# Kernel optimization log

Measured on AMD Instinct MI355X. Metric: run time of the kernel, lower is better.

The kernel has to match this reference:

```python
import math
import jax, jax.numpy as jnp
import numpy as np

B, N, D, H = 2, 8192, 1024, 16


def setup_inputs() -> dict:
    key = jax.random.key(0)
    k1, k2, k3, k4 = jax.random.split(key, 4)
    s = 1.0 / math.sqrt(D)
    return {
        "x": jax.random.normal(k1, (B, N, D), dtype=jnp.float32),
        "W_qk": jax.random.normal(k2, (D, D), dtype=jnp.float32) * s,
        "W_v": jax.random.normal(k3, (D, D), dtype=jnp.float32) * s,
        "W_out": jax.random.normal(k4, (D, D), dtype=jnp.float32) * s,
        "tau": jnp.ones((H, 1, 1), dtype=jnp.float32),
    }


def reference(x, W_qk, W_v, W_out, tau):
    b, n, d = x.shape
    h = H
    dh = d // h
    # QK / V projections (no bias), then to channel-major (B, H, dh, N)
    qk = (x @ W_qk).transpose(0, 2, 1).reshape(b, h, dh, n)
    v = (x @ W_v).transpose(0, 2, 1).reshape(b, h, dh, n)
    # Cross-channel Gram matrix over tokens: (B, H, dh, dh)
    dot = jnp.einsum('bhcn,bhdn->bhcd', qk, qk)
    q2 = jnp.sum(qk * qk, axis=-1)  # (B, H, dh)
    # Negative squared Euclidean distance between channel vectors
    logits = (2.0 * dot - q2[:, :, :, None] - q2[:, :, None, :]) / math.sqrt(max(n, 1))
    logits = logits * tau[None, ...]
    attn = jax.nn.softmax(logits, axis=-1)  # (B, H, dh, dh)
    w = jnp.einsum('bhcd,bhdn->bhcn', attn, v)  # (B, H, dh, N)
    out = w.reshape(b, d, n).transpose(0, 2, 1) @ W_out  # (B, N, D)
    return out
```

## Files before the change

kernel.cpp:

```cpp
#include <hip/hip_runtime.h>
#include <hip/hip_bf16.h>
#include <cstdint>
#include <cstddef>

typedef __bf16 v8bf __attribute__((ext_vector_type(8)));
typedef float  v4f  __attribute__((ext_vector_type(4)));

__device__ __forceinline__ unsigned short f2bf(float f) {
    unsigned int u = __float_as_uint(f);
    u += 0x7fffu + ((u >> 16) & 1u);
    return (unsigned short)(u >> 16);
}

__device__ __forceinline__ void gload_lds16(const unsigned short* g, unsigned short* l) {
    __builtin_amdgcn_global_load_lds(
        (const __attribute__((address_space(1))) unsigned int*)(uintptr_t)g,
        (__attribute__((address_space(3))) unsigned int*)(uintptr_t)l, 16, 0, 0);
}

template<int WRITE_BF16>
__global__ __launch_bounds__(256, 2) void gemm_bt(
    const unsigned short* __restrict__ A,
    const unsigned short* __restrict__ BT,
    void* __restrict__ C,
    int K, int lda, int ldb, int ldc,
    size_t sAz, size_t sBz, size_t sCz,
    int nBlk, int mPerXcd)
{
    __shared__ unsigned short sA[128 * 32];
    __shared__ unsigned short sB[128 * 32];

    const int id = blockIdx.x;
    const int xcd = id & 7;
    int s = id >> 3;
    const int perXcd = mPerXcd * nBlk;
    const int z = s / perXcd;
    s -= z * perXcd;
    const int mB = xcd * mPerXcd + s / nBlk;
    const int nB = s - (s / nBlk) * nBlk;

    const unsigned short* Ab = A + (size_t)z * sAz;
    const unsigned short* Bb = BT + (size_t)z * sBz;

    const int tid  = threadIdx.x;
    const int wv   = tid >> 6;
    const int lane = tid & 63;
    const int quad = lane >> 4;
    const int l16  = lane & 15;
    const size_t bm = (size_t)mB * 128;
    const size_t bn = (size_t)nB * 128;
    const int wm = (wv >> 1) * 64;
    const int wn = (wv & 1) * 64;

    const int ro = tid >> 2;
    const int ko = (((tid & 3) ^ (ro & 3)) << 3);

    const unsigned short* aptr0 = Ab + (bm + ro)      * (size_t)lda + ko;
    const unsigned short* aptr1 = Ab + (bm + ro + 64) * (size_t)lda + ko;
    const unsigned short* bptr0 = Bb + (bn + ro)      * (size_t)ldb + ko;
    const unsigned short* bptr1 = Bb + (bn + ro + 64) * (size_t)ldb + ko;

    unsigned short* sA0 = &sA[wv * 512];
    unsigned short* sA1 = &sA[2048 + wv * 512];
    unsigned short* sB0 = &sB[wv * 512];
    unsigned short* sB1 = &sB[2048 + wv * 512];

    const int sslot = ((quad ^ (l16 & 3)) << 3);

    v4f acc[4][4] = {};

    for (int k0 = 0; k0 < K; k0 += 32) {
        gload_lds16(aptr0 + k0, sA0);
        gload_lds16(aptr1 + k0, sA1);
        gload_lds16(bptr0 + k0, sB0);
        gload_lds16(bptr1 + k0, sB1);
        __syncthreads();

        v8bf af[4], bfr[4];
        #pragma unroll
        for (int t = 0; t < 4; t++) {
            af[t]  = *(const v8bf*)&sA[(size_t)(wm + t * 16 + l16) * 32 + sslot];
            bfr[t] = *(const v8bf*)&sB[(size_t)(wn + t * 16 + l16) * 32 + sslot];
        }

        #pragma unroll
        for (int ti = 0; ti < 4; ti++)
            #pragma unroll
            for (int tj = 0; tj < 4; tj++)
                acc[ti][tj] = __builtin_amdgcn_mfma_f32_16x16x32_bf16(
                    af[ti], bfr[tj], acc[ti][tj], 0, 0, 0);
        __syncthreads();
    }

    if (WRITE_BF16) {
        unsigned short* Cb = (unsigned short*)C + (size_t)z * sCz;
        #pragma unroll
        for (int ti = 0; ti < 4; ti++) {
            const size_t row0 = bm + wm + ti * 16 + quad * 4;
            #pragma unroll
            for (int tj = 0; tj < 4; tj++) {
                const size_t col = bn + wn + tj * 16 + l16;
                #pragma unroll
                for (int r = 0; r < 4; r++)
                    Cb[(row0 + r) * (size_t)ldc + col] = f2bf(acc[ti][tj][r]);
            }
        }
    } else {
        float* Cb = (float*)C + (size_t)z * sCz;
        #pragma unroll
        for (int ti = 0; ti < 4; ti++) {
            const size_t row0 = bm + wm + ti * 16 + quad * 4;
            #pragma unroll
            for (int tj = 0; tj < 4; tj++) {
                const size_t col = bn + wn + tj * 16 + l16;
                #pragma unroll
                for (int r = 0; r < 4; r++)
                    Cb[(row0 + r) * (size_t)ldc + col] = acc[ti][tj][r];
            }
        }
    }
}

__global__ __launch_bounds__(256) void gram_kernel(
    const unsigned short* __restrict__ qk,
    float* __restrict__ partial)
{
    const int bh = blockIdx.x;
    const int split = blockIdx.y;
    const int b = bh >> 4, h = bh & 15;
    const unsigned short* base = qk + (size_t)b * 8192 * 1024 + (size_t)h * 64;
    const int n0 = split * 512;

    __shared__ unsigned short sMT[64 * 136];
    const int tid = threadIdx.x;
    const int wv = tid >> 6, lane = tid & 63, quad = lane >> 4, l16 = lane & 15;

    uint4 pre[4];
    #pragma unroll
    for (int i = 0; i < 4; i++) {
        const int ch = tid + i * 256, tok = ch >> 3, co = (ch & 7) << 3;
        pre[i] = *(const uint4*)(base + (size_t)(n0 + tok) * 1024 + co);
    }

    v4f acc[4] = {};

    for (int chunk = 0; chunk < 4; chunk++) {
        __syncthreads();
        #pragma unroll
        for (int i = 0; i < 4; i++) {
            const int ch = tid + i * 256, tok = ch >> 3, co = (ch & 7) << 3;
            union { uint4 v; unsigned short s8[8]; } u; u.v = pre[i];
            #pragma unroll
            for (int j = 0; j < 8; j++)
                sMT[(size_t)(co + j) * 136 + tok] = u.s8[j];
        }
        __syncthreads();

        if (chunk < 3) {
            const int nb = n0 + (chunk + 1) * 128;
            #pragma unroll
            for (int i = 0; i < 4; i++) {
                const int ch = tid + i * 256, tok = ch >> 3, co = (ch & 7) << 3;
                pre[i] = *(const uint4*)(base + (size_t)(nb + tok) * 1024 + co);
            }
        }

        #pragma unroll
        for (int ks = 0; ks < 4; ks++) {
            const int kb = ks * 32 + quad * 8;
            const v8bf a = *(const v8bf*)&sMT[(size_t)(16 * wv + l16) * 136 + kb];
            #pragma unroll
            for (int t = 0; t < 4; t++) {
                const v8bf bb = *(const v8bf*)&sMT[(size_t)(t * 16 + l16) * 136 + kb];
                acc[t] = __builtin_amdgcn_mfma_f32_16x16x32_bf16(a, bb, acc[t], 0, 0, 0);
            }
        }
    }

    float* outp = partial + ((size_t)split * 32 + bh) * 4096;
    #pragma unroll
    for (int t = 0; t < 4; t++)
        #pragma unroll
        for (int r = 0; r < 4; r++)
            outp[(size_t)(16 * wv + quad * 4 + r) * 64 + t * 16 + l16] = acc[t][r];
}

__global__ __launch_bounds__(256) void softmax_kernel(
    const float* __restrict__ partial,
    const float* __restrict__ tau,
    float* __restrict__ attnT)
{
    const int gw = (int)((blockIdx.x * 256 + threadIdx.x) >> 6);
    const int d = threadIdx.x & 63;
    const int bh = gw >> 6;
    const int c = gw & 63;
    const int h = bh & 15;

    float cd = 0.f, cc = 0.f, dd = 0.f;
    #pragma unroll
    for (int s = 0; s < 16; s++) {
        const float* p = partial + ((size_t)s * 32 + bh) * 4096;
        cd += p[c * 64 + d];
        cc += p[c * 65];
        dd += p[d * 65];
    }
    const float INV_SQRT_N = 0.011048543456039806f;
    const float logit = (2.f * cd - cc - dd) * INV_SQRT_N * tau[h];

    float m = logit;
    #pragma unroll
    for (int off = 32; off > 0; off >>= 1) m = fmaxf(m, __shfl_xor(m, off, 64));
    const float e = __expf(logit - m);
    float sum = e;
    #pragma unroll
    for (int off = 32; off > 0; off >>= 1) sum += __shfl_xor(sum, off, 64);

    attnT[(size_t)bh * 4096 + d * 64 + c] = e / sum;
}

__global__ __launch_bounds__(256) void wefft_kernel(
    const float* __restrict__ attnT,
    const float* __restrict__ Wout,
    unsigned short* __restrict__ weffT)
{
    const int bh = blockIdx.x;
    const int jg = blockIdx.y;
    const int b = bh >> 4, h = bh & 15;

    __shared__ float sAttT[64][65];
    __shared__ float sW[64][65];
    const int tid = threadIdx.x;
    const float* ap = attnT + (size_t)bh * 4096;
    const float* wp = Wout + (size_t)(h * 64) * 1024 + jg * 64;
    for (int i = tid; i < 4096; i += 256) {
        const int r = i >> 6, q = i & 63;
        sAttT[r][q] = ap[i];
        sW[r][q] = wp[(size_t)r * 1024 + q];
    }
    __syncthreads();

    const int dd0 = (tid >> 4) << 2;
    const int j0  = (tid & 15) << 2;
    float acc[4][4] = {};
    for (int cc = 0; cc < 64; cc++) {
        float av[4], wvv[4];
        #pragma unroll
        for (int i = 0; i < 4; i++) av[i] = sAttT[dd0 + i][cc];
        #pragma unroll
        for (int i = 0; i < 4; i++) wvv[i] = sW[cc][j0 + i];
        #pragma unroll
        for (int i = 0; i < 4; i++)
            #pragma unroll
            for (int j = 0; j < 4; j++)
                acc[i][j] += av[i] * wvv[j];
    }

    unsigned short* op = weffT + ((size_t)b * 1024 + jg * 64) * 1024 + h * 64;
    #pragma unroll
    for (int i = 0; i < 4; i++)
        #pragma unroll
        for (int j = 0; j < 4; j++)
            op[(size_t)(j0 + j) * 1024 + dd0 + i] = f2bf(acc[i][j]);
}

__global__ __launch_bounds__(256) void cvt_all_kernel(
    const float* __restrict__ x, const float* __restrict__ Wv,
    const float* __restrict__ Wqk,
    unsigned short* __restrict__ xb, unsigned short* __restrict__ wvb,
    unsigned short* __restrict__ wqkT)
{
    const int bid = blockIdx.x;
    if (bid < 17408) {
        const float* src = (bid < 16384) ? x : Wv;
        unsigned short* dst = (bid < 16384) ? xb : wvb;
        const size_t blk = (bid < 16384) ? bid : (bid - 16384);
        const size_t i = (blk * 256 + threadIdx.x) * 4;
        const float4 v = *(const float4*)(src + i);
        ushort4 o;
        o.x = f2bf(v.x); o.y = f2bf(v.y); o.z = f2bf(v.z); o.w = f2bf(v.w);
        *(ushort4*)(dst + i) = o;
    } else {
        const int t = bid - 17408;
        const int n0 = (t & 31) * 32, k0 = (t >> 5) * 32;
        __shared__ float sT[32][33];
        const int tx = threadIdx.x & 31, ty = threadIdx.x >> 5;
        #pragma unroll
        for (int i = ty; i < 32; i += 8)
            sT[i][tx] = Wqk[(size_t)(k0 + i) * 1024 + n0 + tx];
        __syncthreads();
        #pragma unroll
        for (int i = ty; i < 32; i += 8)
            wqkT[(size_t)(n0 + i) * 1024 + k0 + tx] = f2bf(sT[tx][i]);
    }
}

extern "C" void kernel_launch(void* const* d_in, const int* in_sizes, int n_in,
                              void* d_out, int out_size, void* d_ws, size_t ws_size,
                              hipStream_t stream)
{
    (void)in_sizes; (void)n_in; (void)out_size; (void)ws_size;
    const float* x    = (const float*)d_in[0];
    const float* Wqk  = (const float*)d_in[1];
    const float* Wv   = (const float*)d_in[2];
    const float* Wout = (const float*)d_in[3];
    const float* tau  = (const float*)d_in[4];

    unsigned short* xb     = (unsigned short*)d_ws;
    unsigned short* wqkT   = xb + (size_t)16384 * 1024;
    unsigned short* wvb    = wqkT + (size_t)1024 * 1024;
    unsigned short* qk     = wvb + (size_t)1024 * 1024;
    float*          partial= (float*)(qk + (size_t)16384 * 1024);
    float*          attnT  = partial + (size_t)16 * 32 * 4096;
    unsigned short* weffT  = (unsigned short*)(attnT + (size_t)32 * 4096);
    unsigned short* wfoldT = weffT + (size_t)2 * 1024 * 1024;

    cvt_all_kernel<<<18432, 256, 0, stream>>>(x, Wv, Wqk, xb, wvb, wqkT);

    gemm_bt<1><<<1024, 256, 0, stream>>>(
        xb, wqkT, (void*)qk, 1024, 1024, 1024, 1024, 0, 0, 0, 8, 16);

    gram_kernel<<<dim3(32, 16), 256, 0, stream>>>(qk, partial);
    softmax_kernel<<<512, 256, 0, stream>>>(partial, tau, attnT);
    wefft_kernel<<<dim3(32, 16), 256, 0, stream>>>(attnT, Wout, weffT);

    gemm_bt<1><<<128, 256, 0, stream>>>(
        weffT, wvb, (void*)wfoldT, 1024, 1024, 1024, 1024,
        (size_t)1024 * 1024, 0, (size_t)1024 * 1024, 8, 1);

    gemm_bt<0><<<1024, 256, 0, stream>>>(
        xb, wfoldT, d_out, 1024, 1024, 1024, 1024,
        (size_t)8192 * 1024, (size_t)1024 * 1024, (size_t)8192 * 1024, 8, 8);
}
```

Before: 264.2 us.

## Add 256x256-tile 8-wave GEMM with quadrant-interleaved prefetch for large projections

Adds a new GEMM kernel using 256x256 output tiles, 512 threads, and a double-buffered 128 KB LDS ring. LDS reads and the next global-to-LDS loads are interleaved across four MFMA quadrants, with setprio raised around the MFMA groups. The two large GEMMs over 16384x1024 (QK projection and final output) switch to it, cutting their grids from 1024 to 256 blocks. The larger tiles raise arithmetic intensity and reduce redundant loads, at the cost of fewer blocks in flight, many barriers, and heavy register use.

```diff
diff --git a/kernel.cpp b/kernel.cpp
--- a/kernel.cpp
+++ b/kernel.cpp
@@ -120,6 +120,208 @@
         }
     }
 }
+
+#define MFMA_QUAD(MH, NH)                                                     \
+    do {                                                                      \
+        __builtin_amdgcn_s_setprio(1);                                        \
+        _Pragma("unroll")                                                     \
+        for (int mi = 0; mi < 4; ++mi) {                                      \
+            _Pragma("unroll")                                                 \
+            for (int ni = 0; ni < 2; ++ni) {                                  \
+                acc[(MH)*4 + mi][(NH)*2 + ni] =                               \
+                    __builtin_amdgcn_mfma_f32_16x16x32_bf16(                  \
+                        aF[mi][0], bF[NH][ni][0],                             \
+                        acc[(MH)*4 + mi][(NH)*2 + ni], 0, 0, 0);              \
+                acc[(MH)*4 + mi][(NH)*2 + ni] =                               \
+                    __builtin_amdgcn_mfma_f32_16x16x32_bf16(                  \
+                        aF[mi][1], bF[NH][ni][1],                             \
+                        acc[(MH)*4 + mi][(NH)*2 + ni], 0, 0, 0);              \
+            }                                                                 \
+        }                                                                     \
+        __builtin_amdgcn_s_setprio(0);                                        \
+    } while (0)
+
+template<int WRITE_BF16>
+__global__ __launch_bounds__(512, 2) void gemm256_bt(
+    const unsigned short* __restrict__ A,
+    const unsigned short* __restrict__ BT,
+    void* __restrict__ C,
+    int K, int lda, int ldb, int ldc,
+    size_t sAz, size_t sBz, size_t sCz,
+    int nBlk, int mPerXcd)
+{
+    __shared__ unsigned short sm[65536];
+
+    const int id = blockIdx.x;
+    const int xcd = id & 7;
+    int s = id >> 3;
+    const int perXcd = mPerXcd * nBlk;
+    const int z = s / perXcd;
+    s -= z * perXcd;
+    const int mB = xcd * mPerXcd + s / nBlk;
+    const int nB = s - (s / nBlk) * nBlk;
+
+    const unsigned short* Ab = A + (size_t)z * sAz;
+    const unsigned short* Bb = BT + (size_t)z * sBz;
+
+    const int tid  = threadIdx.x;
+    const int wv   = tid >> 6;
+    const int lane = tid & 63;
+    const int quad = lane >> 4;
+    const int l16  = lane & 15;
+    const int wm   = wv >> 2;
+    const int wn   = wv & 3;
+
+    const size_t bm = (size_t)mB * 256;
+    const size_t bn = (size_t)nB * 256;
+
+    const int r0   = tid >> 3;
+    const int slog = (tid & 7) ^ (r0 & 7);
+    const unsigned short* aP = Ab + (bm + r0) * (size_t)lda + slog * 8;
+    const unsigned short* bP = Bb + (bn + r0) * (size_t)ldb + slog * 8;
+
+    const int stA = wv * 512;
+
+    const int soff0 = (quad ^ (l16 & 7)) * 8;
+    const int arow0 = (wm * 64 + l16) * 64 + soff0;
+    const int brow0 = (wn * 32 + l16) * 64 + soff0;
+
+    v4f  acc[8][4] = {};
+    v8bf aF[4][2];
+    v8bf bF[2][2][2];
+
+    const int NT = K >> 6;
+
+    {
+        gload_lds16(aP,                sm + stA);
+        gload_lds16(aP + 64 * lda,     sm + stA + 4096);
+        gload_lds16(bP,                sm + 32768 + stA);
+        gload_lds16(bP + 64 * ldb,     sm + 32768 + stA + 4096);
+        gload_lds16(bP + 128 * ldb,    sm + 32768 + 8192 + stA);
+        gload_lds16(bP + 192 * ldb,    sm + 32768 + 8192 + stA + 4096);
+        gload_lds16(aP + 128 * lda,    sm + 8192 + stA);
+        gload_lds16(aP + 192 * lda,    sm + 8192 + stA + 4096);
+        if (NT > 1) {
+            gload_lds16(aP + 64,                 sm + 16384 + stA);
+            gload_lds16(aP + 64 * lda + 64,      sm + 16384 + stA + 4096);
+            gload_lds16(bP + 64,                 sm + 32768 + 16384 + stA);
+            gload_lds16(bP + 64 * ldb + 64,      sm + 32768 + 16384 + stA + 4096);
+            gload_lds16(bP + 128 * ldb + 64,     sm + 32768 + 16384 + 8192 + stA);
+            gload_lds16(bP + 192 * ldb + 64,     sm + 32768 + 16384 + 8192 + stA + 4096);
+            asm volatile("s_waitcnt vmcnt(6)" ::: "memory");
+        } else {
+            asm volatile("s_waitcnt vmcnt(0)" ::: "memory");
+        }
+        __builtin_amdgcn_s_barrier();
+    }
+
+    for (int t = 0; t < NT; ++t) {
+        const int p = t & 1;
+        const unsigned short* sa = sm + p * 16384;
+        const unsigned short* sb = sm + 32768 + p * 16384;
+        unsigned short* dq = sm + (p ^ 1) * 16384;
+        unsigned short* dp = sm + p * 16384;
+        const int kk1 = (t + 1) * 64;
+        const int kk2 = (t + 2) * 64;
+
+        #pragma unroll
+        for (int mi = 0; mi < 4; ++mi) {
+            aF[mi][0] = *(const v8bf*)(sa + (arow0 + mi * 1024));
+            aF[mi][1] = *(const v8bf*)(sa + ((arow0 + mi * 1024) ^ 32));
+        }
+        #pragma unroll
+        for (int ni = 0; ni < 2; ++ni) {
+            bF[0][ni][0] = *(const v8bf*)(sb + (brow0 + ni * 1024));
+            bF[0][ni][1] = *(const v8bf*)(sb + ((brow0 + ni * 1024) ^ 32));
+        }
+        if (t + 1 < NT) {
+            gload_lds16(aP + 128 * lda + kk1, dq + 8192 + stA);
+            gload_lds16(aP + 192 * lda + kk1, dq + 8192 + stA + 4096);
+        }
+        __builtin_amdgcn_s_barrier();
+        asm volatile("s_waitcnt lgkmcnt(0)" ::: "memory");
+        MFMA_QUAD(0, 0);
+        __builtin_amdgcn_s_barrier();
+
+        #pragma unroll
+        for (int ni = 0; ni < 2; ++ni) {
+            bF[1][ni][0] = *(const v8bf*)(sb + 8192 + (brow0 + ni * 1024));
+            bF[1][ni][1] = *(const v8bf*)(sb + 8192 + ((brow0 + ni * 1024) ^ 32));
+        }
+        if (t + 2 < NT) {
+            gload_lds16(aP + kk2,            dp + stA);
+            gload_lds16(aP + 64 * lda + kk2, dp + stA + 4096);
+        }
+        __builtin_amdgcn_s_barrier();
+        asm volatile("s_waitcnt lgkmcnt(0)" ::: "memory");
+        MFMA_QUAD(0, 1);
+        __builtin_amdgcn_s_barrier();
+
+        #pragma unroll
+        for (int mi = 0; mi < 4; ++mi) {
+            aF[mi][0] = *(const v8bf*)(sa + 8192 + (arow0 + mi * 1024));
+            aF[mi][1] = *(const v8bf*)(sa + 8192 + ((arow0 + mi * 1024) ^ 32));
+        }
+        if (t + 2 < NT) {
+            gload_lds16(bP + kk2,            dp + 32768 + stA);
+            gload_lds16(bP + 64 * ldb + kk2, dp + 32768 + stA + 4096);
+        }
+        __builtin_amdgcn_s_barrier();
+        asm volatile("s_waitcnt lgkmcnt(0)" ::: "memory");
+        MFMA_QUAD(1, 1);
+        __builtin_amdgcn_s_barrier();
+
+        if (t + 2 < NT) {
+            gload_lds16(bP + 128 * ldb + kk2, dp + 32768 + 8192 + stA);
+            gload_lds16(bP + 192 * ldb + kk2, dp + 32768 + 8192 + stA + 4096);
+            asm volatile("s_waitcnt vmcnt(6)" ::: "memory");
+        } else {
+            asm volatile("s_waitcnt vmcnt(0)" ::: "memory");
+        }
+        __builtin_amdgcn_s_barrier();
+        MFMA_QUAD(1, 0);
+        __builtin_amdgcn_s_barrier();
+    }
+
+    if (WRITE_BF16) {
+        unsigned short* Cb = (unsigned short*)C + (size_t)z * sCz;
+        #pragma unroll
+        for (int mh = 0; mh < 2; ++mh)
+            #pragma unroll
+            for (int mi = 0; mi < 4; ++mi) {
+                const size_t row0 = bm + mh * 128 + wm * 64 + mi * 16 + quad * 4;
+                #pragma unroll
+                for (int nh = 0; nh < 2; ++nh)
+                    #pragma unroll
+                    for (int ni = 0; ni < 2; ++ni) {
+                        const size_t col = bn + nh * 128 + wn * 32 + ni * 16 + l16;
+                        #pragma unroll
+                        for (int r = 0; r < 4; ++r)
+                            Cb[(row0 + r) * (size_t)ldc + col] =
+                                f2bf(acc[mh * 4 + mi][nh * 2 + ni][r]);
+                    }
+            }
+    } else {
+        float* Cb = (float*)C + (size_t)z * sCz;
+        #pragma unroll
+        for (int mh = 0; mh < 2; ++mh)
+            #pragma unroll
+            for (int mi = 0; mi < 4; ++mi) {
+                const size_t row0 = bm + mh * 128 + wm * 64 + mi * 16 + quad * 4;
+                #pragma unroll
+                for (int nh = 0; nh < 2; ++nh)
+                    #pragma unroll
+                    for (int ni = 0; ni < 2; ++ni) {
+                        const size_t col = bn + nh * 128 + wn * 32 + ni * 16 + l16;
+                        #pragma unroll
+                        for (int r = 0; r < 4; ++r)
+                            Cb[(row0 + r) * (size_t)ldc + col] =
+                                acc[mh * 4 + mi][nh * 2 + ni][r];
+                    }
+            }
+    }
+}
+#undef MFMA_QUAD
 
 __global__ __launch_bounds__(256) void gram_kernel(
     const unsigned short* __restrict__ qk,
@@ -316,8 +518,8 @@
 
     cvt_all_kernel<<<18432, 256, 0, stream>>>(x, Wv, Wqk, xb, wvb, wqkT);
 
-    gemm_bt<1><<<1024, 256, 0, stream>>>(
-        xb, wqkT, (void*)qk, 1024, 1024, 1024, 1024, 0, 0, 0, 8, 16);
+    gemm256_bt<1><<<256, 512, 0, stream>>>(
+        xb, wqkT, (void*)qk, 1024, 1024, 1024, 1024, 0, 0, 0, 4, 8);
 
     gram_kernel<<<dim3(32, 16), 256, 0, stream>>>(qk, partial);
     softmax_kernel<<<512, 256, 0, stream>>>(partial, tau, attnT);
@@ -327,7 +529,7 @@
         weffT, wvb, (void*)wfoldT, 1024, 1024, 1024, 1024,
         (size_t)1024 * 1024, 0, (size_t)1024 * 1024, 8, 1);
 
-    gemm_bt<0><<<1024, 256, 0, stream>>>(
+    gemm256_bt<0><<<256, 512, 0, stream>>>(
         xb, wfoldT, d_out, 1024, 1024, 1024, 1024,
-        (size_t)8192 * 1024, (size_t)1024 * 1024, (size_t)8192 * 1024, 8, 8);
-}
+        (size_t)8192 * 1024, (size_t)1024 * 1024, (size_t)8192 * 1024, 4, 4);
+}
```

Result: no change. 261.6 us (-1.0%).
